# Kernel tuning notes

Hardware: AMD Instinct MI355X
Metric: run time of the kernel (lower is better)

Reference implementation:

```python
import jax, jax.numpy as jnp
import numpy as np

EPS = 1e-5
GROUPS = 8


def _gn_per_channel(x, w, b):
    # GroupNorm with num_groups == num_channels: per-channel instance norm over (h, w)
    m = x.mean(axis=(2, 3), keepdims=True)
    v = x.var(axis=(2, 3), keepdims=True)  # biased var, matches torch GroupNorm
    xn = (x - m) * jax.lax.rsqrt(v + EPS)
    return xn * w[None, :, None, None] + b[None, :, None, None]


def setup_inputs() -> dict:
    key = jax.random.key(0)
    k0, k1 = jax.random.split(key)
    b, c, h, w = 16, 512, 64, 64
    cg = c // GROUPS          # 64 per-group channels
    half = cg // 2            # 32
    x = jax.random.normal(k0, (b, c, h, w), jnp.float32)
    conv1x1_w = jax.random.normal(k1, (cg, cg), jnp.float32) / np.float32(np.sqrt(cg))
    conv1x1_b = jnp.zeros((cg,), jnp.float32)
    gn_w = jnp.ones((cg,), jnp.float32)
    gn_b = jnp.zeros((cg,), jnp.float32)
    gn1_w = jnp.ones((half,), jnp.float32)
    gn1_b = jnp.zeros((half,), jnp.float32)
    cweight = jnp.zeros((1, half, 1, 1), jnp.float32)
    cbias = jnp.ones((1, half, 1, 1), jnp.float32)
    sweight = jnp.zeros((1, half, 1, 1), jnp.float32)
    sbias = jnp.ones((1, half, 1, 1), jnp.float32)
    return {"x": x, "conv1x1_w": conv1x1_w, "conv1x1_b": conv1x1_b,
            "gn_w": gn_w, "gn_b": gn_b, "gn1_w": gn1_w, "gn1_b": gn1_b,
            "cweight": cweight, "cbias": cbias, "sweight": sweight, "sbias": sbias}


def reference(x, conv1x1_w, conv1x1_b, gn_w, gn_b, gn1_w, gn1_b,
              cweight, cbias, sweight, sbias):
    b, c, h, w = x.shape
    g = GROUPS
    cg = c // g
    half = cg // 2
    bg = b * g
    gx = x.reshape(bg, cg, h, w)  # group_x

    # coordinate-attention branch: pool along W and H
    x_h = gx.mean(axis=3, keepdims=True)                      # (bg, cg, h, 1)
    x_w = gx.mean(axis=2, keepdims=True).transpose(0, 1, 3, 2)  # (bg, cg, w, 1)
    hw_cat = jnp.concatenate([x_h, x_w], axis=2)              # (bg, cg, h+w, 1)
    hw = jnp.einsum('oi,bilk->bolk', conv1x1_w, hw_cat) + conv1x1_b[None, :, None, None]
    xh = hw[:, :, :h]                       # (bg, cg, h, 1)
    xw = hw[:, :, h:].transpose(0, 1, 3, 2)  # (bg, cg, 1, w)
    x1 = _gn_per_channel(gx * jax.nn.sigmoid(xh) * jax.nn.sigmoid(xw), gn_w, gn_b)

    # shuffle-attention branch on chunked channels
    x0, x1b = gx[:, :half], gx[:, half:]
    xc = x0.mean(axis=(2, 3), keepdims=True)                  # (bg, half, 1, 1)
    x_channel = x0 * jax.nn.sigmoid(cweight * xc + cbias)
    xs = _gn_per_channel(x1b, gn1_w, gn1_b)
    x_spatial = x1b * jax.nn.sigmoid(sweight * xs + sbias)
    out = jnp.concatenate([x_channel, x_spatial], axis=1)     # (bg, cg, h, w)
    # channel shuffle with g=2
    x2 = out.reshape(bg, 2, half, h, w).transpose(0, 2, 1, 3, 4).reshape(bg, cg, h, w)

    # cross-branch attention weights via small batched matmuls
    x11 = jax.nn.softmax(x1.mean(axis=(2, 3)).reshape(bg, 1, cg), axis=-1)
    x21 = jax.nn.softmax(x2.mean(axis=(2, 3)).reshape(bg, 1, cg), axis=-1)
    x12 = x2.reshape(bg, cg, h * w)
    x22 = x1.reshape(bg, cg, h * w)
    weights = (jnp.matmul(x11, x12) + jnp.matmul(x21, x22)).reshape(bg, 1, h, w)
    return (gx * jax.nn.sigmoid(weights)).reshape(b, c, h, w)
```

## Files before the change

### kernel.cpp

```cpp
#include <hip/hip_runtime.h>
#include <math.h>

#define EPSV 1e-5f

typedef float vfloat4 __attribute__((ext_vector_type(4)));

__device__ __forceinline__ float fast_rcp(float x) {
#if __has_builtin(__builtin_amdgcn_rcpf)
    return __builtin_amdgcn_rcpf(x);
#else
    return 1.0f / x;
#endif
}

__device__ __forceinline__ float sigmoidf_(float x) {
    return fast_rcp(1.0f + __expf(-x));
}

__global__ __launch_bounds__(256) void k_statsA(
    const float* __restrict__ x,
    float* __restrict__ rowmean,
    float* __restrict__ colmean,
    float* __restrict__ meanA,
    float* __restrict__ varA)
{
    const int t = threadIdx.x, l = t & 63, wv = t >> 6;
    const int plane = blockIdx.x * 4 + wv;
    const float4* p4 = (const float4*)(x + (size_t)plane * 4096);
    float c0 = 0.f, c1 = 0.f, c2 = 0.f, c3 = 0.f, s = 0.f, ss = 0.f;
#pragma unroll 8
    for (int k = 0; k < 16; ++k) {
        float4 v = p4[k * 64 + l];
        float rp = v.x + v.y + v.z + v.w;
        s += rp;
        ss += v.x * v.x + v.y * v.y + v.z * v.z + v.w * v.w;
        c0 += v.x; c1 += v.y; c2 += v.z; c3 += v.w;
#pragma unroll
        for (int m = 8; m >= 1; m >>= 1) rp += __shfl_xor(rp, m, 16);
        if ((l & 15) == 0)
            rowmean[(size_t)plane * 64 + k * 4 + (l >> 4)] = rp * (1.f / 64.f);
    }
#pragma unroll
    for (int m = 32; m >= 16; m >>= 1) {
        c0 += __shfl_xor(c0, m); c1 += __shfl_xor(c1, m);
        c2 += __shfl_xor(c2, m); c3 += __shfl_xor(c3, m);
    }
    if (l < 16) {
        float4 cm = { c0 * (1.f / 64.f), c1 * (1.f / 64.f),
                      c2 * (1.f / 64.f), c3 * (1.f / 64.f) };
        ((float4*)(colmean + (size_t)plane * 64))[l] = cm;
    }
#pragma unroll
    for (int m = 32; m >= 1; m >>= 1) { s += __shfl_xor(s, m); ss += __shfl_xor(ss, m); }
    if (l == 0) {
        float mn = s * (1.f / 4096.f);
        meanA[plane] = mn;
        varA[plane] = ss * (1.f / 4096.f) - mn * mn;
    }
}

__global__ __launch_bounds__(256) void k_conv(
    const float* __restrict__ W, const float* __restrict__ Wb,
    const float* __restrict__ rowmean, const float* __restrict__ colmean,
    float* __restrict__ shg, float* __restrict__ swg)
{
    int blk = blockIdx.x;
    int bg = blk >> 1, rc = blk & 1;
    const float* rm = (rc ? colmean : rowmean) + (size_t)bg * 4096;
    float* outp = (rc ? swg : shg) + (size_t)bg * 4096;
    int t = threadIdx.x, lane = t & 63, wv = t >> 6;
    float r[64];
#pragma unroll
    for (int i = 0; i < 64; ++i) r[i] = rm[i * 64 + lane];
    for (int j = 0; j < 16; ++j) {
        int c = wv * 16 + j;
        float acc = Wb[c];
#pragma unroll
        for (int i = 0; i < 64; ++i)
            acc = fmaf(W[c * 64 + i], r[i], acc);
        outp[c * 64 + lane] = sigmoidf_(acc);
    }
}

__global__ __launch_bounds__(256) void k_statsC(
    const float* __restrict__ x,
    const float* __restrict__ shg, const float* __restrict__ swg,
    const float* __restrict__ meanA, const float* __restrict__ varA,
    const float* __restrict__ swt, const float* __restrict__ sbs,
    const float* __restrict__ gn1w, const float* __restrict__ gn1b,
    float* __restrict__ meanT, float* __restrict__ varT,
    float* __restrict__ spat)
{
    const int t = threadIdx.x, l = t & 63, wv = t >> 6;
    const int plane = blockIdx.x * 4 + wv;
    const int cch = plane & 63, bgc = plane >> 6;
    const float4* p4 = (const float4*)(x + (size_t)plane * 4096);
    float4 sw4 = ((const float4*)(swg + (size_t)plane * 64))[l & 15];
    float a = 0.f, bb = 0.f;
    const bool spatial = (cch >= 32);
    if (spatial) {
        int i = cch - 32;
        float mu = meanA[plane];
        float r2 = rsqrtf(varA[plane] + EPSV);
        a = swt[i] * gn1w[i] * r2;
        bb = swt[i] * (gn1b[i] - mu * r2 * gn1w[i]) + sbs[i];
    }
    float st = 0.f, sst = 0.f, ssp = 0.f;
#pragma unroll 8
    for (int k = 0; k < 16; ++k) {
        float4 v = p4[k * 64 + l];
        float sh = shg[(size_t)plane * 64 + k * 4 + (l >> 4)];
        float t0 = v.x * sh * sw4.x;
        float t1 = v.y * sh * sw4.y;
        float t2 = v.z * sh * sw4.z;
        float t3 = v.w * sh * sw4.w;
        st += t0 + t1 + t2 + t3;
        sst += t0 * t0 + t1 * t1 + t2 * t2 + t3 * t3;
        if (spatial) {
            ssp += v.x * sigmoidf_(fmaf(a, v.x, bb))
                 + v.y * sigmoidf_(fmaf(a, v.y, bb))
                 + v.z * sigmoidf_(fmaf(a, v.z, bb))
                 + v.w * sigmoidf_(fmaf(a, v.w, bb));
        }
    }
#pragma unroll
    for (int m = 32; m >= 1; m >>= 1) {
        st += __shfl_xor(st, m); sst += __shfl_xor(sst, m); ssp += __shfl_xor(ssp, m);
    }
    if (l == 0) {
        float mn = st * (1.f / 4096.f);
        meanT[plane] = mn;
        varT[plane] = sst * (1.f / 4096.f) - mn * mn;
        if (spatial) spat[bgc * 32 + (cch - 32)] = ssp * (1.f / 4096.f);
    }
}

__global__ __launch_bounds__(256, 4) void k_final2(
    const float* __restrict__ x,
    const float* __restrict__ shg, const float* __restrict__ swg,
    const float* __restrict__ meanA, const float* __restrict__ varA,
    const float* __restrict__ meanT, const float* __restrict__ varT,
    const float* __restrict__ spat,
    const float* __restrict__ gnw, const float* __restrict__ gnb,
    const float* __restrict__ gn1w, const float* __restrict__ gn1b,
    const float* __restrict__ cwt, const float* __restrict__ cbs,
    const float* __restrict__ swt, const float* __restrict__ sbs,
    float* __restrict__ outp)
{
    const int blk = blockIdx.x;
    const int bg = blk >> 4, band = blk & 15;
    const int h0 = band << 2;
    const int t = threadIdx.x, l = t & 63, wv = t >> 6;

    __shared__ float swf[64 * 64];
    __shared__ float shf[64 * 4];
    __shared__ float eL[64], gL[32], dL[32], aL[32], bL[32];
    __shared__ float kS;
    __shared__ float4 red[4][64];
    __shared__ float4 sig4[64];

#pragma unroll
    for (int j = 0; j < 4; ++j) {
        int f = t + 256 * j;
        ((float4*)swf)[f] = ((const float4*)(swg + (size_t)bg * 4096))[f];
    }
    {
        int c = t >> 2, r = t & 3;
        shf[t] = shg[(size_t)bg * 4096 + c * 64 + h0 + r];
    }

    if (wv == 0) {
        const int c = l;
        size_t idx = (size_t)bg * 64 + c;
        float Aj = 0.f, Bj = 0.f, scj = 0.f;
        if (c < 32) {
            float xc = meanA[idx];
            scj = sigmoidf_(fmaf(cwt[c], xc, cbs[c]));
            Aj = scj * xc;
            Bj = spat[bg * 32 + c];
        }
        float As = __shfl(Aj, c >> 1);
        float Bs = __shfl(Bj, c >> 1);
        float v2 = (c & 1) ? Bs : As;
        float v1 = gnb[c];
        float mx = v1;
#pragma unroll
        for (int m = 32; m >= 1; m >>= 1) mx = fmaxf(mx, __shfl_xor(mx, m));
        float e1 = __expf(v1 - mx);
        float s1 = e1;
#pragma unroll
        for (int m = 32; m >= 1; m >>= 1) s1 += __shfl_xor(s1, m);
        float x11 = e1 / s1;
        mx = v2;
#pragma unroll
        for (int m = 32; m >= 1; m >>= 1) mx = fmaxf(mx, __shfl_xor(mx, m));
        float e2 = __expf(v2 - mx);
        float s2 = e2;
#pragma unroll
        for (int m = 32; m >= 1; m >>= 1) s2 += __shfl_xor(s2, m);
        float x21 = e2 / s2;

        float mT = meanT[idx];
        float rt = rsqrtf(varT[idx] + EPSV);
        float e_c = x21 * gnw[c] * rt;
        float kp = x21 * (gnb[c] - gnw[c] * rt * mT);
#pragma unroll
        for (int m = 32; m >= 1; m >>= 1) kp += __shfl_xor(kp, m);
        float x11e = __shfl(x11, (2 * c) & 63);
        float x11o = __shfl(x11, (2 * c + 1) & 63);
        eL[c] = e_c;
        if (c == 0) kS = kp;
        if (c < 32) {
            gL[c] = x11e * scj;
            dL[c] = x11o;
            size_t idx2 = (size_t)bg * 64 + 32 + c;
            float mu = meanA[idx2];
            float r2 = rsqrtf(varA[idx2] + EPSV);
            aL[c] = swt[c] * gn1w[c] * r2;
            bL[c] = swt[c] * (gn1b[c] - mu * r2 * gn1w[c]) + sbs[c];
        }
    }
    __syncthreads();

    const int r = l >> 4, qc = l & 15;
    const float* xp = x + (size_t)bg * 262144 + (size_t)(h0 + r) * 64 + qc * 4;
    const int c0 = wv * 16;
    float4 xc[16];
    float4 part = {0.f, 0.f, 0.f, 0.f};
    if (wv < 2) {
#pragma unroll
        for (int cc = 0; cc < 16; ++cc) {
            int c = c0 + cc;
            float4 v = *(const float4*)(xp + (size_t)c * 4096);
            xc[cc] = v;
            float ce = eL[c] * shf[c * 4 + r];
            float gc = gL[c];
            float4 s4 = *(const float4*)&swf[c * 64 + qc * 4];
            part.x = fmaf(fmaf(ce, s4.x, gc), v.x, part.x);
            part.y = fmaf(fmaf(ce, s4.y, gc), v.y, part.y);
            part.z = fmaf(fmaf(ce, s4.z, gc), v.z, part.z);
            part.w = fmaf(fmaf(ce, s4.w, gc), v.w, part.w);
        }
    } else {
#pragma unroll
        for (int cc = 0; cc < 16; ++cc) {
            int c = c0 + cc;
            int i = c - 32;
            float4 v = *(const float4*)(xp + (size_t)c * 4096);
            xc[cc] = v;
            float ce = eL[c] * shf[c * 4 + r];
            float ai = aL[i], bi = bL[i], di = dL[i];
            float4 s4 = *(const float4*)&swf[c * 64 + qc * 4];
            part.x = fmaf(ce * s4.x, v.x, part.x);
            part.x = fmaf(di * v.x, sigmoidf_(fmaf(ai, v.x, bi)), part.x);
            part.y = fmaf(ce * s4.y, v.y, part.y);
            part.y = fmaf(di * v.y, sigmoidf_(fmaf(ai, v.y, bi)), part.y);
            part.z = fmaf(ce * s4.z, v.z, part.z);
            part.z = fmaf(di * v.z, sigmoidf_(fmaf(ai, v.z, bi)), part.z);
            part.w = fmaf(ce * s4.w, v.w, part.w);
            part.w = fmaf(di * v.w, sigmoidf_(fmaf(ai, v.w, bi)), part.w);
        }
    }
    red[wv][l] = part;
    __syncthreads();
    if (wv == 0) {
        float4 p0 = red[0][l], p1 = red[1][l], p2 = red[2][l], p3 = red[3][l];
        float K = kS;
        float4 sgv;
        sgv.x = sigmoidf_(K + p0.x + p1.x + p2.x + p3.x);
        sgv.y = sigmoidf_(K + p0.y + p1.y + p2.y + p3.y);
        sgv.z = sigmoidf_(K + p0.z + p1.z + p2.z + p3.z);
        sgv.w = sigmoidf_(K + p0.w + p1.w + p2.w + p3.w);
        sig4[l] = sgv;
    }
    __syncthreads();
    const float4 sg = sig4[l];
    float* op = outp + (xp - x);
#pragma unroll
    for (int cc = 0; cc < 16; ++cc) {
        int c = c0 + cc;
        float4 v = xc[cc];
        vfloat4 o = { v.x * sg.x, v.y * sg.y, v.z * sg.z, v.w * sg.w };
        __builtin_nontemporal_store(o, (vfloat4*)(op + (size_t)c * 4096));
    }
}

extern "C" void kernel_launch(void* const* d_in, const int* in_sizes, int n_in,
                              void* d_out, int out_size, void* d_ws, size_t ws_size,
                              hipStream_t stream) {
    (void)in_sizes; (void)n_in; (void)out_size; (void)ws_size;
    const float* x    = (const float*)d_in[0];
    const float* W    = (const float*)d_in[1];
    const float* Wb   = (const float*)d_in[2];
    const float* gnw  = (const float*)d_in[3];
    const float* gnb  = (const float*)d_in[4];
    const float* gn1w = (const float*)d_in[5];
    const float* gn1b = (const float*)d_in[6];
    const float* cwt  = (const float*)d_in[7];
    const float* cbs  = (const float*)d_in[8];
    const float* swt  = (const float*)d_in[9];
    const float* sbs  = (const float*)d_in[10];
    float* out = (float*)d_out;
    float* ws = (float*)d_ws;

    float* rowmean = ws;
    float* colmean = rowmean + 524288;
    float* shg     = colmean + 524288;
    float* swg     = shg + 524288;
    float* meanA   = swg + 524288;
    float* varA    = meanA + 8192;
    float* meanT   = varA + 8192;
    float* varT    = meanT + 8192;
    float* spat    = varT + 8192;

    k_statsA<<<2048, 256, 0, stream>>>(x, rowmean, colmean, meanA, varA);
    k_conv<<<256, 256, 0, stream>>>(W, Wb, rowmean, colmean, shg, swg);
    k_statsC<<<2048, 256, 0, stream>>>(x, shg, swg, meanA, varA, swt, sbs, gn1w, gn1b,
                                       meanT, varT, spat);
    k_final2<<<2048, 256, 0, stream>>>(x, shg, swg, meanA, varA, meanT, varT, spat,
                                       gnw, gnb, gn1w, gn1b, cwt, cbs, swt, sbs, out);
}
```

Before: 321.4 us.

## Fuse conv, second stats pass and softmax coefficients into one per-group kernel

Merges the 1x1 conv gate kernel, the second statistics pass over x and the per-group softmax/coefficient setup into a single kernel, with one 1024-thread block per batch-group. Gates stay in shared memory for the stats pass, and the final kernel now just loads precomputed coefficients instead of recomputing them in every one of its 16 band blocks. This removes a launch and the global round-trip of the stats. The cost is that the full read of x in the stats pass now runs on only 128 large blocks at one block per CU, which may leave much of the GPU idle and limit bandwidth.

```diff
diff --git a/kernel.cpp b/kernel.cpp
--- a/kernel.cpp
+++ b/kernel.cpp
@@ -59,115 +59,97 @@
     }
 }
 
-__global__ __launch_bounds__(256) void k_conv(
+__global__ __launch_bounds__(1024, 1) void k_bcd(
+    const float* __restrict__ x,
     const float* __restrict__ W, const float* __restrict__ Wb,
     const float* __restrict__ rowmean, const float* __restrict__ colmean,
-    float* __restrict__ shg, float* __restrict__ swg)
-{
-    int blk = blockIdx.x;
-    int bg = blk >> 1, rc = blk & 1;
-    const float* rm = (rc ? colmean : rowmean) + (size_t)bg * 4096;
-    float* outp = (rc ? swg : shg) + (size_t)bg * 4096;
-    int t = threadIdx.x, lane = t & 63, wv = t >> 6;
-    float r[64];
-#pragma unroll
-    for (int i = 0; i < 64; ++i) r[i] = rm[i * 64 + lane];
-    for (int j = 0; j < 16; ++j) {
-        int c = wv * 16 + j;
-        float acc = Wb[c];
-#pragma unroll
-        for (int i = 0; i < 64; ++i)
-            acc = fmaf(W[c * 64 + i], r[i], acc);
-        outp[c * 64 + lane] = sigmoidf_(acc);
-    }
-}
-
-__global__ __launch_bounds__(256) void k_statsC(
-    const float* __restrict__ x,
-    const float* __restrict__ shg, const float* __restrict__ swg,
     const float* __restrict__ meanA, const float* __restrict__ varA,
-    const float* __restrict__ swt, const float* __restrict__ sbs,
-    const float* __restrict__ gn1w, const float* __restrict__ gn1b,
-    float* __restrict__ meanT, float* __restrict__ varT,
-    float* __restrict__ spat)
-{
-    const int t = threadIdx.x, l = t & 63, wv = t >> 6;
-    const int plane = blockIdx.x * 4 + wv;
-    const int cch = plane & 63, bgc = plane >> 6;
-    const float4* p4 = (const float4*)(x + (size_t)plane * 4096);
-    float4 sw4 = ((const float4*)(swg + (size_t)plane * 64))[l & 15];
-    float a = 0.f, bb = 0.f;
-    const bool spatial = (cch >= 32);
-    if (spatial) {
-        int i = cch - 32;
-        float mu = meanA[plane];
-        float r2 = rsqrtf(varA[plane] + EPSV);
-        a = swt[i] * gn1w[i] * r2;
-        bb = swt[i] * (gn1b[i] - mu * r2 * gn1w[i]) + sbs[i];
-    }
-    float st = 0.f, sst = 0.f, ssp = 0.f;
-#pragma unroll 8
-    for (int k = 0; k < 16; ++k) {
-        float4 v = p4[k * 64 + l];
-        float sh = shg[(size_t)plane * 64 + k * 4 + (l >> 4)];
-        float t0 = v.x * sh * sw4.x;
-        float t1 = v.y * sh * sw4.y;
-        float t2 = v.z * sh * sw4.z;
-        float t3 = v.w * sh * sw4.w;
-        st += t0 + t1 + t2 + t3;
-        sst += t0 * t0 + t1 * t1 + t2 * t2 + t3 * t3;
-        if (spatial) {
-            ssp += v.x * sigmoidf_(fmaf(a, v.x, bb))
-                 + v.y * sigmoidf_(fmaf(a, v.y, bb))
-                 + v.z * sigmoidf_(fmaf(a, v.z, bb))
-                 + v.w * sigmoidf_(fmaf(a, v.w, bb));
-        }
-    }
-#pragma unroll
-    for (int m = 32; m >= 1; m >>= 1) {
-        st += __shfl_xor(st, m); sst += __shfl_xor(sst, m); ssp += __shfl_xor(ssp, m);
-    }
-    if (l == 0) {
-        float mn = st * (1.f / 4096.f);
-        meanT[plane] = mn;
-        varT[plane] = sst * (1.f / 4096.f) - mn * mn;
-        if (spatial) spat[bgc * 32 + (cch - 32)] = ssp * (1.f / 4096.f);
-    }
-}
-
-__global__ __launch_bounds__(256, 4) void k_final2(
-    const float* __restrict__ x,
-    const float* __restrict__ shg, const float* __restrict__ swg,
-    const float* __restrict__ meanA, const float* __restrict__ varA,
-    const float* __restrict__ meanT, const float* __restrict__ varT,
-    const float* __restrict__ spat,
     const float* __restrict__ gnw, const float* __restrict__ gnb,
     const float* __restrict__ gn1w, const float* __restrict__ gn1b,
     const float* __restrict__ cwt, const float* __restrict__ cbs,
     const float* __restrict__ swt, const float* __restrict__ sbs,
-    float* __restrict__ outp)
+    float* __restrict__ shg, float* __restrict__ swg,
+    float* __restrict__ eArr, float* __restrict__ gArr,
+    float* __restrict__ dArr, float* __restrict__ aArr,
+    float* __restrict__ bArr, float* __restrict__ kArr)
 {
-    const int blk = blockIdx.x;
-    const int bg = blk >> 4, band = blk & 15;
-    const int h0 = band << 2;
+    const int bg = blockIdx.x;
     const int t = threadIdx.x, l = t & 63, wv = t >> 6;
-
-    __shared__ float swf[64 * 64];
-    __shared__ float shf[64 * 4];
-    __shared__ float eL[64], gL[32], dL[32], aL[32], bL[32];
-    __shared__ float kS;
-    __shared__ float4 red[4][64];
-    __shared__ float4 sig4[64];
+    __shared__ float rmL[2][64][64];
+    __shared__ float gateL[2][64][64];
+    __shared__ float mTl[64], vTl[64], spl[32];
 
 #pragma unroll
     for (int j = 0; j < 4; ++j) {
-        int f = t + 256 * j;
-        ((float4*)swf)[f] = ((const float4*)(swg + (size_t)bg * 4096))[f];
-    }
+        int idx = t + 1024 * j;
+        ((float*)rmL[0])[idx] = rowmean[(size_t)bg * 4096 + idx];
+        ((float*)rmL[1])[idx] = colmean[(size_t)bg * 4096 + idx];
+    }
+    __syncthreads();
+
     {
-        int c = t >> 2, r = t & 3;
-        shf[t] = shg[(size_t)bg * 4096 + c * 64 + h0 + r];
-    }
+        const int rc = wv >> 3, cbase = (wv & 7) * 8, pos = l;
+        float r[64];
+#pragma unroll
+        for (int i = 0; i < 64; ++i) r[i] = rmL[rc][i][pos];
+#pragma unroll
+        for (int j = 0; j < 8; ++j) {
+            int c = cbase + j;
+            float acc = Wb[c];
+#pragma unroll
+            for (int i = 0; i < 64; ++i) acc = fmaf(W[c * 64 + i], r[i], acc);
+            float g = sigmoidf_(acc);
+            gateL[rc][c][pos] = g;
+            (rc ? swg : shg)[(size_t)bg * 4096 + c * 64 + pos] = g;
+        }
+    }
+    __syncthreads();
+
+#pragma unroll
+    for (int pi = 0; pi < 4; ++pi) {
+        const int p = wv * 4 + pi;
+        const int plane = bg * 64 + p;
+        const float4* p4 = (const float4*)(x + (size_t)plane * 4096);
+        float4 sw4 = ((float4*)&gateL[1][p][0])[l & 15];
+        float a = 0.f, bb = 0.f;
+        const bool spatial = (p >= 32);
+        if (spatial) {
+            int i = p - 32;
+            float mu = meanA[plane];
+            float r2 = rsqrtf(varA[plane] + EPSV);
+            a = swt[i] * gn1w[i] * r2;
+            bb = swt[i] * (gn1b[i] - mu * r2 * gn1w[i]) + sbs[i];
+        }
+        float st = 0.f, sst = 0.f, ssp = 0.f;
+#pragma unroll 8
+        for (int k = 0; k < 16; ++k) {
+            float4 v = p4[k * 64 + l];
+            float sh = gateL[0][p][k * 4 + (l >> 4)];
+            float t0 = v.x * sh * sw4.x;
+            float t1 = v.y * sh * sw4.y;
+            float t2 = v.z * sh * sw4.z;
+            float t3 = v.w * sh * sw4.w;
+            st += t0 + t1 + t2 + t3;
+            sst += t0 * t0 + t1 * t1 + t2 * t2 + t3 * t3;
+            if (spatial) {
+                ssp += v.x * sigmoidf_(fmaf(a, v.x, bb))
+                     + v.y * sigmoidf_(fmaf(a, v.y, bb))
+                     + v.z * sigmoidf_(fmaf(a, v.z, bb))
+                     + v.w * sigmoidf_(fmaf(a, v.w, bb));
+            }
+        }
+#pragma unroll
+        for (int m = 32; m >= 1; m >>= 1) {
+            st += __shfl_xor(st, m); sst += __shfl_xor(sst, m); ssp += __shfl_xor(ssp, m);
+        }
+        if (l == 0) {
+            float mn = st * (1.f / 4096.f);
+            mTl[p] = mn;
+            vTl[p] = sst * (1.f / 4096.f) - mn * mn;
+            if (spatial) spl[p - 32] = ssp * (1.f / 4096.f);
+        }
+    }
+    __syncthreads();
 
     if (wv == 0) {
         const int c = l;
@@ -177,7 +159,7 @@
             float xc = meanA[idx];
             scj = sigmoidf_(fmaf(cwt[c], xc, cbs[c]));
             Aj = scj * xc;
-            Bj = spat[bg * 32 + c];
+            Bj = spl[c];
         }
         float As = __shfl(Aj, c >> 1);
         float Bs = __shfl(Bj, c >> 1);
@@ -200,26 +182,62 @@
         for (int m = 32; m >= 1; m >>= 1) s2 += __shfl_xor(s2, m);
         float x21 = e2 / s2;
 
-        float mT = meanT[idx];
-        float rt = rsqrtf(varT[idx] + EPSV);
+        float mT = mTl[c];
+        float rt = rsqrtf(vTl[c] + EPSV);
         float e_c = x21 * gnw[c] * rt;
         float kp = x21 * (gnb[c] - gnw[c] * rt * mT);
 #pragma unroll
         for (int m = 32; m >= 1; m >>= 1) kp += __shfl_xor(kp, m);
         float x11e = __shfl(x11, (2 * c) & 63);
         float x11o = __shfl(x11, (2 * c + 1) & 63);
-        eL[c] = e_c;
-        if (c == 0) kS = kp;
+        eArr[idx] = e_c;
+        if (c == 0) kArr[bg] = kp;
         if (c < 32) {
-            gL[c] = x11e * scj;
-            dL[c] = x11o;
+            gArr[bg * 32 + c] = x11e * scj;
+            dArr[bg * 32 + c] = x11o;
             size_t idx2 = (size_t)bg * 64 + 32 + c;
             float mu = meanA[idx2];
             float r2 = rsqrtf(varA[idx2] + EPSV);
-            aL[c] = swt[c] * gn1w[c] * r2;
-            bL[c] = swt[c] * (gn1b[c] - mu * r2 * gn1w[c]) + sbs[c];
-        }
-    }
+            aArr[bg * 32 + c] = swt[c] * gn1w[c] * r2;
+            bArr[bg * 32 + c] = swt[c] * (gn1b[c] - mu * r2 * gn1w[c]) + sbs[c];
+        }
+    }
+}
+
+__global__ __launch_bounds__(256, 4) void k_final3(
+    const float* __restrict__ x,
+    const float* __restrict__ shg, const float* __restrict__ swg,
+    const float* __restrict__ eArr, const float* __restrict__ gArr,
+    const float* __restrict__ dArr, const float* __restrict__ aArr,
+    const float* __restrict__ bArr, const float* __restrict__ kArr,
+    float* __restrict__ outp)
+{
+    const int blk = blockIdx.x;
+    const int bg = blk >> 4, band = blk & 15;
+    const int h0 = band << 2;
+    const int t = threadIdx.x, l = t & 63, wv = t >> 6;
+
+    __shared__ float swf[64 * 64];
+    __shared__ float shf[64 * 4];
+    __shared__ float eL[64], gL[32], dL[32], aL[32], bL[32];
+    __shared__ float4 red[4][64];
+    __shared__ float4 sig4[64];
+
+#pragma unroll
+    for (int j = 0; j < 4; ++j) {
+        int f = t + 256 * j;
+        ((float4*)swf)[f] = ((const float4*)(swg + (size_t)bg * 4096))[f];
+    }
+    {
+        int c = t >> 2, r = t & 3;
+        shf[t] = shg[(size_t)bg * 4096 + c * 64 + h0 + r];
+    }
+    if (t < 64)       eL[t]       = eArr[(size_t)bg * 64 + t];
+    else if (t < 96)  gL[t - 64]  = gArr[bg * 32 + t - 64];
+    else if (t < 128) dL[t - 96]  = dArr[bg * 32 + t - 96];
+    else if (t < 160) aL[t - 128] = aArr[bg * 32 + t - 128];
+    else if (t < 192) bL[t - 160] = bArr[bg * 32 + t - 160];
+    const float K = kArr[bg];
     __syncthreads();
 
     const int r = l >> 4, qc = l & 15;
@@ -265,7 +283,6 @@
     __syncthreads();
     if (wv == 0) {
         float4 p0 = red[0][l], p1 = red[1][l], p2 = red[2][l], p3 = red[3][l];
-        float K = kS;
         float4 sgv;
         sgv.x = sigmoidf_(K + p0.x + p1.x + p2.x + p3.x);
         sgv.y = sigmoidf_(K + p0.y + p1.y + p2.y + p3.y);
@@ -309,14 +326,17 @@
     float* swg     = shg + 524288;
     float* meanA   = swg + 524288;
     float* varA    = meanA + 8192;
-    float* meanT   = varA + 8192;
-    float* varT    = meanT + 8192;
-    float* spat    = varT + 8192;
+    float* eArr    = varA + 8192;
+    float* gArr    = eArr + 8192;
+    float* dArr    = gArr + 4096;
+    float* aArr    = dArr + 4096;
+    float* bArr    = aArr + 4096;
+    float* kArr    = bArr + 4096;
 
     k_statsA<<<2048, 256, 0, stream>>>(x, rowmean, colmean, meanA, varA);
-    k_conv<<<256, 256, 0, stream>>>(W, Wb, rowmean, colmean, shg, swg);
-    k_statsC<<<2048, 256, 0, stream>>>(x, shg, swg, meanA, varA, swt, sbs, gn1w, gn1b,
-                                       meanT, varT, spat);
-    k_final2<<<2048, 256, 0, stream>>>(x, shg, swg, meanA, varA, meanT, varT, spat,
-                                       gnw, gnb, gn1w, gn1b, cwt, cbs, swt, sbs, out);
-}
+    k_bcd<<<128, 1024, 0, stream>>>(x, W, Wb, rowmean, colmean, meanA, varA,
+                                    gnw, gnb, gn1w, gn1b, cwt, cbs, swt, sbs,
+                                    shg, swg, eArr, gArr, dArr, aArr, bArr, kArr);
+    k_final3<<<2048, 256, 0, stream>>>(x, shg, swg, eArr, gArr, dArr, aArr, bArr,
+                                       kArr, out);
+}
```

New measurement: 327.7 us. No clear change (+2.0%).
